# Kernel tuning notes

Hardware: AMD Instinct MI355X
Metric: run time of the kernel (lower is better)

The kernel has to match this reference:

```python
import jax, jax.numpy as jnp
import numpy as np

MASK_H = 7   # mask_height from init
MASK_W = 2   # mask_width from init
SUPPRESS = 0.9


def setup_inputs() -> dict:
    key = jax.random.key(0)
    k1, k2, k3 = jax.random.split(key, 3)
    B, C, H, W = 64, 512, 28, 28
    x = jax.random.normal(k1, (B, C, H, W), dtype=jnp.float32)
    mask_y = jax.random.randint(k2, (B, C), 0, H - MASK_H + 1, dtype=jnp.int32)
    mask_x = jax.random.randint(k3, (B, C), 0, W - MASK_W + 1, dtype=jnp.int32)
    return {"x": x, "mask_y": mask_y, "mask_x": mask_x}


def reference(x, mask_y, mask_x):
    # x: [B,C,H,W]; mask_y/mask_x: [B,C] top-left corners of the random block.
    B, C, H, W = x.shape
    # Peak mask (helperb1): 1 where the per-channel max is attained (incl. ties).
    max_val = jnp.max(x, axis=(2, 3), keepdims=True)          # [B,C,1,1]
    peak = x == max_val                                        # [B,C,H,W] bool
    # Random block mask (create_mask): MASK_H x MASK_W block per channel.
    rows = jnp.arange(H)                                       # [H]
    cols = jnp.arange(W)                                       # [W]
    y0 = mask_y[..., None]                                     # [B,C,1]
    x0 = mask_x[..., None]
    row_in = (rows >= y0) & (rows < y0 + MASK_H)               # [B,C,H]
    col_in = (cols >= x0) & (cols < x0 + MASK_W)               # [B,C,W]
    rand = row_in[..., :, None] & col_in[..., None, :]         # [B,C,H,W]
    # Join: clamp(b1 + b2, 0, 1) == logical or; suppress masked cells by 0.9.
    mask = (peak | rand).astype(x.dtype)
    return x - SUPPRESS * x * mask
```

## Files before the change

kernel.cpp:

```cpp
#include <hip/hip_runtime.h>


constexpr int Hdim = 28;
constexpr int Wdim = 28;
constexpr int HW = Hdim * Wdim;
constexpr int NF4 = HW / 4;
constexpr float SUPPRESS = 0.9f;

typedef float f4 __attribute__((ext_vector_type(4)));

__global__ __launch_bounds__(256) void selectdropmax_kernel(
    const float* __restrict__ x,
    const int* __restrict__ mask_y,
    const int* __restrict__ mask_x,
    float* __restrict__ out,
    int nch)
{
    const int gtid = blockIdx.x * blockDim.x + threadIdx.x;
    const int ch   = gtid >> 6;
    const int lane = threadIdx.x & 63;
    if (ch >= nch) return;

    const f4* __restrict__ xp = reinterpret_cast<const f4*>(x) + (size_t)ch * NF4;
    f4* __restrict__ op       = reinterpret_cast<f4*>(out) + (size_t)ch * NF4;

    const bool extra = (lane < (NF4 - 192));
    f4 v0 = xp[lane];
    f4 v1 = xp[lane + 64];
    f4 v2 = xp[lane + 128];
    f4 v3 = (f4){0.f, 0.f, 0.f, 0.f};
    if (extra) v3 = xp[lane + 192];

    float m = fmaxf(fmaxf(v0.x, v0.y), fmaxf(v0.z, v0.w));
    m = fmaxf(m, fmaxf(fmaxf(v1.x, v1.y), fmaxf(v1.z, v1.w)));
    m = fmaxf(m, fmaxf(fmaxf(v2.x, v2.y), fmaxf(v2.z, v2.w)));
    if (extra) m = fmaxf(m, fmaxf(fmaxf(v3.x, v3.y), fmaxf(v3.z, v3.w)));

    #pragma unroll
    for (int off = 32; off > 0; off >>= 1)
        m = fmaxf(m, __shfl_xor(m, off, 64));

    const int y0 = mask_y[ch];
    const int x0 = mask_x[ch];

    auto proc = [&](f4 v, int f4idx) -> f4 {
        f4 res;
        const int base = f4idx * 4;
        #pragma unroll
        for (int j = 0; j < 4; ++j) {
            const float val = v[j];
            const int idx = base + j;
            const int h = idx / Wdim;
            const int w = idx - h * Wdim;
            const bool inblk = (h >= y0) & (h < y0 + 7) & (w >= x0) & (w < x0 + 2);
            const bool msk = (val == m) | inblk;
            const float t = SUPPRESS * val;
            res[j] = msk ? (val - t) : val;
        }
        return res;
    };

    f4 r0 = proc(v0, lane);
    f4 r1 = proc(v1, lane + 64);
    f4 r2 = proc(v2, lane + 128);
    __builtin_nontemporal_store(r0, &op[lane]);
    __builtin_nontemporal_store(r1, &op[lane + 64]);
    __builtin_nontemporal_store(r2, &op[lane + 128]);
    if (extra) {
        f4 r3 = proc(v3, lane + 192);
        __builtin_nontemporal_store(r3, &op[lane + 192]);
    }
}

extern "C" void kernel_launch(void* const* d_in, const int* in_sizes, int n_in,
                              void* d_out, int out_size, void* d_ws, size_t ws_size,
                              hipStream_t stream) {
    const float* x      = (const float*)d_in[0];
    const int*   mask_y = (const int*)d_in[1];
    const int*   mask_x = (const int*)d_in[2];
    float*       out    = (float*)d_out;

    const int nch = in_sizes[1];
    const int waves_per_block = 4;
    const int nblocks = (nch + waves_per_block - 1) / waves_per_block;

    hipLaunchKernelGGL(selectdropmax_kernel,
                       dim3(nblocks), dim3(256), 0, stream,
                       x, mask_y, mask_x, out, nch);
}
```

Measured before the change: 35.33 us.

## Use persistent grid-stride waves with double-buffered channel prefetch

Changes the launch from one wave per channel to a fixed grid of 2048 blocks, where each wave loops over channels with a grid stride. Each wave loads the next channel's data into a second register set while it processes and stores the current one, so memory latency overlaps with compute. This cuts per-wave launch overhead. In exchange it uses more registers, which may lower occupancy, and it may run fewer waves in flight than the original one-wave-per-channel launch.

After: 36.34 us. 2.9% more time.

```diff
diff --git a/kernel.cpp b/kernel.cpp
--- a/kernel.cpp
+++ b/kernel.cpp
@@ -1,9 +1,8 @@
 #include <hip/hip_runtime.h>
 
 
-constexpr int Hdim = 28;
 constexpr int Wdim = 28;
-constexpr int HW = Hdim * Wdim;
+constexpr int HW = 28 * 28;
 constexpr int NF4 = HW / 4;
 constexpr float SUPPRESS = 0.9f;
 
@@ -16,59 +15,84 @@
     float* __restrict__ out,
     int nch)
 {
-    const int gtid = blockIdx.x * blockDim.x + threadIdx.x;
-    const int ch   = gtid >> 6;
-    const int lane = threadIdx.x & 63;
-    if (ch >= nch) return;
+    const int lane  = threadIdx.x & 63;
+    const int wid   = blockIdx.x * (blockDim.x >> 6) + (threadIdx.x >> 6);
+    const int nwave = gridDim.x * (blockDim.x >> 6);
+    const bool extra = (lane < (NF4 - 192));
 
-    const f4* __restrict__ xp = reinterpret_cast<const f4*>(x) + (size_t)ch * NF4;
-    f4* __restrict__ op       = reinterpret_cast<f4*>(out) + (size_t)ch * NF4;
+    const f4* __restrict__ xv = reinterpret_cast<const f4*>(x);
+    f4* __restrict__ ov       = reinterpret_cast<f4*>(out);
 
-    const bool extra = (lane < (NF4 - 192));
-    f4 v0 = xp[lane];
-    f4 v1 = xp[lane + 64];
-    f4 v2 = xp[lane + 128];
-    f4 v3 = (f4){0.f, 0.f, 0.f, 0.f};
-    if (extra) v3 = xp[lane + 192];
-
-    float m = fmaxf(fmaxf(v0.x, v0.y), fmaxf(v0.z, v0.w));
-    m = fmaxf(m, fmaxf(fmaxf(v1.x, v1.y), fmaxf(v1.z, v1.w)));
-    m = fmaxf(m, fmaxf(fmaxf(v2.x, v2.y), fmaxf(v2.z, v2.w)));
-    if (extra) m = fmaxf(m, fmaxf(fmaxf(v3.x, v3.y), fmaxf(v3.z, v3.w)));
-
-    #pragma unroll
-    for (int off = 32; off > 0; off >>= 1)
-        m = fmaxf(m, __shfl_xor(m, off, 64));
-
-    const int y0 = mask_y[ch];
-    const int x0 = mask_x[ch];
-
-    auto proc = [&](f4 v, int f4idx) -> f4 {
-        f4 res;
-        const int base = f4idx * 4;
-        #pragma unroll
-        for (int j = 0; j < 4; ++j) {
-            const float val = v[j];
-            const int idx = base + j;
-            const int h = idx / Wdim;
-            const int w = idx - h * Wdim;
-            const bool inblk = (h >= y0) & (h < y0 + 7) & (w >= x0) & (w < x0 + 2);
-            const bool msk = (val == m) | inblk;
-            const float t = SUPPRESS * val;
-            res[j] = msk ? (val - t) : val;
-        }
-        return res;
+    auto load_ch = [&](int c, f4& v0, f4& v1, f4& v2, f4& v3, int& y0, int& x0) {
+        const f4* __restrict__ xp = xv + (size_t)c * NF4;
+        v0 = xp[lane];
+        v1 = xp[lane + 64];
+        v2 = xp[lane + 128];
+        if (extra) v3 = xp[lane + 192];
+        y0 = mask_y[c];
+        x0 = mask_x[c];
     };
 
-    f4 r0 = proc(v0, lane);
-    f4 r1 = proc(v1, lane + 64);
-    f4 r2 = proc(v2, lane + 128);
-    __builtin_nontemporal_store(r0, &op[lane]);
-    __builtin_nontemporal_store(r1, &op[lane + 64]);
-    __builtin_nontemporal_store(r2, &op[lane + 128]);
-    if (extra) {
-        f4 r3 = proc(v3, lane + 192);
-        __builtin_nontemporal_store(r3, &op[lane + 192]);
+    auto proc_store = [&](int c, f4 v0, f4 v1, f4 v2, f4 v3, int y0, int x0) {
+        float m = fmaxf(fmaxf(v0.x, v0.y), fmaxf(v0.z, v0.w));
+        m = fmaxf(m, fmaxf(fmaxf(v1.x, v1.y), fmaxf(v1.z, v1.w)));
+        m = fmaxf(m, fmaxf(fmaxf(v2.x, v2.y), fmaxf(v2.z, v2.w)));
+        if (extra) m = fmaxf(m, fmaxf(fmaxf(v3.x, v3.y), fmaxf(v3.z, v3.w)));
+        #pragma unroll
+        for (int off = 32; off > 0; off >>= 1)
+            m = fmaxf(m, __shfl_xor(m, off, 64));
+
+        auto proc = [&](f4 v, int f4idx) -> f4 {
+            f4 res;
+            const int base = f4idx * 4;
+            #pragma unroll
+            for (int j = 0; j < 4; ++j) {
+                const float val = v[j];
+                const int idx = base + j;
+                const int h = idx / Wdim;
+                const int w = idx - h * Wdim;
+                const bool inblk = (h >= y0) & (h < y0 + 7) & (w >= x0) & (w < x0 + 2);
+                const bool msk = (val == m) | inblk;
+                const float t = SUPPRESS * val;
+                res[j] = msk ? (val - t) : val;
+            }
+            return res;
+        };
+
+        f4* __restrict__ op = ov + (size_t)c * NF4;
+        f4 r0 = proc(v0, lane);
+        f4 r1 = proc(v1, lane + 64);
+        f4 r2 = proc(v2, lane + 128);
+        __builtin_nontemporal_store(r0, &op[lane]);
+        __builtin_nontemporal_store(r1, &op[lane + 64]);
+        __builtin_nontemporal_store(r2, &op[lane + 128]);
+        if (extra) {
+            f4 r3 = proc(v3, lane + 192);
+            __builtin_nontemporal_store(r3, &op[lane + 192]);
+        }
+    };
+
+    f4 a0, a1, a2, a3 = (f4){0,0,0,0};
+    f4 b0, b1, b2, b3 = (f4){0,0,0,0};
+    int ay, ax, by, bx;
+
+    int ch = wid;
+    if (ch >= nch) return;
+    load_ch(ch, a0, a1, a2, a3, ay, ax);
+
+    for (;;) {
+        const int chB = ch + nwave;
+        const bool haveB = chB < nch;
+        if (haveB) load_ch(chB, b0, b1, b2, b3, by, bx);
+        proc_store(ch, a0, a1, a2, a3, ay, ax);
+        if (!haveB) return;
+
+        const int chC = chB + nwave;
+        const bool haveC = chC < nch;
+        if (haveC) load_ch(chC, a0, a1, a2, a3, ay, ax);
+        proc_store(chB, b0, b1, b2, b3, by, bx);
+        if (!haveC) return;
+        ch = chC;
     }
 }
 
@@ -81,8 +105,9 @@
     float*       out    = (float*)d_out;
 
     const int nch = in_sizes[1];
-    const int waves_per_block = 4;
-    const int nblocks = (nch + waves_per_block - 1) / waves_per_block;
+    int nblocks = 2048;
+    const int max_needed = (nch + 3) / 4;
+    if (nblocks > max_needed) nblocks = max_needed;
 
     hipLaunchKernelGGL(selectdropmax_kernel,
                        dim3(nblocks), dim3(256), 0, stream,
```
